# Performance work log

Hardware: AMD Instinct MI355X
Metric: run time of the kernel (lower is better)

Reference implementation:

```python
import jax, jax.numpy as jnp
import numpy as np

B, N, D, H, QP, VP = 2, 2048, 64, 4, 4, 4
DH = D // H  # 16
CUTOFF = 10.0
NEG = -1e9  # stand-in for -inf in masked_fill (identical softmax output, NaN-safe)


def _linear_params(key, din, dout):
    kw, kb = jax.random.split(key)
    W = jax.random.normal(kw, (din, dout), jnp.float32) / np.sqrt(din)
    b = jax.random.normal(kb, (dout,), jnp.float32) * 0.01
    return W, b


def setup_inputs() -> dict:
    key = jax.random.key(0)
    ks = jax.random.split(key, 10)
    features = jax.random.normal(ks[0], (B, N, D), jnp.float32)
    coords = jax.random.uniform(ks[1], (B, N, 3), jnp.float32) * 30.0  # ~protein-scale box (Angstroms)
    Wq, bq = _linear_params(ks[2], D, D)
    Wk, bk = _linear_params(ks[3], D, D)
    Wv, bv = _linear_params(ks[4], D, D)
    Wqp, bqp = _linear_params(ks[5], D, H * QP * 3)
    Wkp, bkp = _linear_params(ks[6], D, H * QP * 3)
    Wvp, bvp = _linear_params(ks[7], D, H * VP * 3)
    Wo, bo = _linear_params(ks[8], D + H * VP * 3, D)
    w_c = jnp.ones((H,), jnp.float32)
    w_l = jnp.ones((H,), jnp.float32)
    return dict(features=features, coords=coords, Wq=Wq, bq=bq, Wk=Wk, bk=bk,
                Wv=Wv, bv=bv, Wqp=Wqp, bqp=bqp, Wkp=Wkp, bkp=bkp,
                Wvp=Wvp, bvp=bvp, Wo=Wo, bo=bo, w_c=w_c, w_l=w_l)


def reference(features, coords, Wq, bq, Wk, bk, Wv, bv,
              Wqp, bqp, Wkp, bkp, Wvp, bvp, Wo, bo, w_c, w_l):
    b, n, _ = features.shape
    # cutoff edge mask (SE3Encoder: dist > cutoff is masked)
    d2 = jnp.sum((coords[:, :, None, :] - coords[:, None, :, :]) ** 2, axis=-1)  # (b,n,n)
    edge_mask = jnp.sqrt(jnp.maximum(d2, 0.0)) > CUTOFF

    q = (features @ Wq + bq).reshape(b, n, H, DH)
    k = (features @ Wk + bk).reshape(b, n, H, DH)
    v = (features @ Wv + bv).reshape(b, n, H, DH)
    qp = (features @ Wqp + bqp).reshape(b, n, H, QP, 3) + coords[:, :, None, None, :]
    kp = (features @ Wkp + bkp).reshape(b, n, H, QP, 3) + coords[:, :, None, None, :]
    vp = (features @ Wvp + bvp).reshape(b, n, H, VP, 3) + coords[:, :, None, None, :]

    linear_attn = jnp.einsum('bihd,bjhd->bhij', q, k) * (DH ** -0.5)
    # sum_{p,d} (qp - kp)^2 = |qp|^2 + |kp|^2 - 2 qp.kp, avoiding (b,n,n,H,P,3) tensor
    qsq = jnp.transpose(jnp.sum(qp ** 2, axis=(-1, -2)), (0, 2, 1))  # (b,h,i)
    ksq = jnp.transpose(jnp.sum(kp ** 2, axis=(-1, -2)), (0, 2, 1))  # (b,h,j)
    cross = jnp.einsum('bihpd,bjhpd->bhij', qp, kp)
    point_attn = -0.5 * (qsq[:, :, :, None] + ksq[:, :, None, :] - 2.0 * cross)

    wl = jax.nn.softplus(w_l)[None, :, None, None]
    wc = jax.nn.softplus(w_c)[None, :, None, None]
    attn = wl * linear_attn + wc * point_attn
    attn = jnp.where(edge_mask[:, None, :, :], NEG, attn)
    attn = jax.nn.softmax(attn, axis=-1)

    out_linear = jnp.einsum('bhij,bjhd->bihd', attn, v).reshape(b, n, -1)
    out_points = jnp.einsum('bhij,bjhpd->bihpd', attn, vp).reshape(b, n, -1)
    out = jnp.concatenate([out_linear, out_points], axis=-1)
    return out @ Wo + bo
```

## Files before the change

### kernel.cpp

```cpp
#include <hip/hip_runtime.h>
#include <hip/hip_bf16.h>

typedef __hip_bfloat16 bf16;
typedef unsigned int uint32;
typedef __attribute__((ext_vector_type(8))) short bf16x8;
typedef __attribute__((ext_vector_type(4))) float f32x4;

#define BB 2
#define NN 2048
#define CENTER 15.0f

#define QT_OFF   16u
#define KT_OFF   786448u
#define VT_OFF   1572880u
#define CQ_OFF   1802256u
#define SB_OFF   1806352u
#define PAR_OFF  2281488u

__device__ __forceinline__ float b2f(bf16 x) { return __bfloat162float(x); }

__device__ __forceinline__ float ldm(const void* p, size_t i, int mode) {
  return mode ? ((const float*)p)[i] : b2f(((const bf16*)p)[i]);
}

__device__ __forceinline__ float softplus_f(float x) {
  return (x > 20.f) ? x : log1pf(__expf(x));
}

__device__ __forceinline__ unsigned pk2(float a, float b) {
  union { __hip_bfloat162 v; unsigned u; } cv;
  cv.v.x = __float2bfloat16(a); cv.v.y = __float2bfloat16(b);
  return cv.u;
}
__device__ __forceinline__ float2 upk2(unsigned u) {
  union { unsigned u; __hip_bfloat162 v; } cv; cv.u = u;
  return make_float2(__bfloat162float(cv.v.x), __bfloat162float(cv.v.y));
}
__device__ __forceinline__ unsigned short f2bu(float x) {
  union { bf16 b; unsigned short u; } c; c.b = __float2bfloat16(x); return c.u;
}
__device__ __forceinline__ float lo_part(float x) {
  return x - __bfloat162float(__float2bfloat16(x));
}

__device__ float qslot(int h, int s, const float* spro, const float* cc,
                       float wl, float wc) {
  if (s < 16) return wl * spro[h * 16 + s];
  if (s < 28) return wc * spro[192 + h * 12 + (s - 16)];
  if (s < 32) return 0.f;
  if (s < 44) return wc * spro[192 + h * 12 + (s - 32)];
  if (s < 56) return lo_part(wc * spro[192 + h * 12 + (s - 44)]);
  if (s < 64) return 0.f;
  if (s < 67) return cc[s - 64];
  if (s < 70) return cc[s - 67];
  if (s < 73) return lo_part(cc[s - 70]);
  return 0.f;
}
__device__ float kslot(int h, int s, const float* spro, const float* cc) {
  if (s < 16) return spro[64 + h * 16 + s];
  if (s < 28) return spro[240 + h * 12 + (s - 16)];
  if (s < 32) return 0.f;
  if (s < 44) return lo_part(spro[240 + h * 12 + (s - 32)]);
  if (s < 56) return spro[240 + h * 12 + (s - 44)];
  if (s < 64) return 0.f;
  if (s < 67) return cc[s - 64];
  if (s < 70) return lo_part(cc[s - 67]);
  if (s < 73) return cc[s - 70];
  return 0.f;
}

__global__ __launch_bounds__(512) void proj_kernel(
    const void* feat, const void* coords,
    const void* Wq,  const void* bq,  const void* Wk,  const void* bk,
    const void* Wv,  const void* bv,  const void* Wqp, const void* bqp,
    const void* Wkp, const void* bkp, const void* Wvp, const void* bvp,
    const void* w_c, const void* w_l, float* ws)
{
  const int t = threadIdx.x;
  const int row0 = blockIdx.x * 4;
  const int b = row0 >> 11;
  __shared__ int scnt;
  __shared__ float sfT[64 * 4];
  __shared__ float spro[4][336];

  if (t == 0) scnt = 0;
  __syncthreads();
  {
    const unsigned short uv = ((const unsigned short*)feat)[t];
    const unsigned e = (uv >> 7) & 0xFFu;
    const unsigned long long bl = __ballot(e >= 0xC0u);
    if ((t & 63) == 0) atomicAdd(&scnt, (int)__popcll(bl));
  }
  __syncthreads();
  const int mode = (scnt > 16) ? 1 : 0;

  if (t < 256) {
    const int rr = t >> 6, f = t & 63;
    sfT[f * 4 + rr] = ldm(feat, (size_t)(row0 + rr) * 64 + f, mode);
  }
  __syncthreads();

  if (t < 336) {
    const void *W, *bias; int odim, c, cls, ofs;
    if (t < 64)       { W = Wq;  bias = bq;  odim = 64; c = t;       cls = 0; ofs = 0; }
    else if (t < 128) { W = Wk;  bias = bk;  odim = 64; c = t - 64;  cls = 1; ofs = 64; }
    else if (t < 192) { W = Wv;  bias = bv;  odim = 64; c = t - 128; cls = 2; ofs = 128; }
    else if (t < 240) { W = Wqp; bias = bqp; odim = 48; c = t - 192; cls = 3; ofs = 192; }
    else if (t < 288) { W = Wkp; bias = bkp; odim = 48; c = t - 240; cls = 4; ofs = 240; }
    else              { W = Wvp; bias = bvp; odim = 48; c = t - 288; cls = 5; ofs = 288; }
    const float bb = ldm(bias, c, mode);
    float a0 = bb, a1 = bb, a2 = bb, a3 = bb;
    if (mode) {
      const float* Wf = (const float*)W;
      #pragma unroll 8
      for (int f = 0; f < 64; ++f) {
        const float wf = Wf[(size_t)f * odim + c];
        const float4 fv = *(const float4*)(sfT + f * 4);
        a0 = fmaf(fv.x, wf, a0); a1 = fmaf(fv.y, wf, a1);
        a2 = fmaf(fv.z, wf, a2); a3 = fmaf(fv.w, wf, a3);
      }
    } else {
      const bf16* Wb = (const bf16*)W;
      #pragma unroll 8
      for (int f = 0; f < 64; ++f) {
        const float wf = b2f(Wb[(size_t)f * odim + c]);
        const float4 fv = *(const float4*)(sfT + f * 4);
        a0 = fmaf(fv.x, wf, a0); a1 = fmaf(fv.y, wf, a1);
        a2 = fmaf(fv.z, wf, a2); a3 = fmaf(fv.w, wf, a3);
      }
    }
    float av[4] = {a0, a1, a2, a3};
    #pragma unroll
    for (int rr = 0; rr < 4; ++rr) {
      float acc = av[rr];
      if (cls >= 3) {
        acc += ldm(coords, (size_t)(row0 + rr) * 3 + (c % 3), mode);
        if (cls == 3 || cls == 4) acc -= CENTER;
      }
      spro[rr][ofs + c] = acc;
    }
  }
  __syncthreads();

  if (t < 384) {
    const bool isq = (t < 192);
    const int per = isq ? t : t - 192;
    const int h = per / 48, w = per - h * 48;
    const float wl = softplus_f(ldm(w_l, h, mode)) * 0.25f;
    const float wc = softplus_f(ldm(w_c, h, mode));
    uint32* tab = (uint32*)(ws + (isq ? QT_OFF : KT_OFF));
    #pragma unroll 1
    for (int rr = 0; rr < 4; ++rr) {
      const int row = row0 + rr, i = row & 2047;
      float cc[3];
      cc[0] = ldm(coords, (size_t)row * 3 + 0, mode) - CENTER;
      cc[1] = ldm(coords, (size_t)row * 3 + 1, mode) - CENTER;
      cc[2] = ldm(coords, (size_t)row * 3 + 2, mode) - CENTER;
      const float* sp = spro[rr];
      float a0, a1;
      if (isq) { a0 = qslot(h, 2 * w, sp, cc, wl, wc);
                 a1 = qslot(h, 2 * w + 1, sp, cc, wl, wc); }
      else     { a0 = kslot(h, 2 * w, sp, cc);
                 a1 = kslot(h, 2 * w + 1, sp, cc); }
      tab[((size_t)(b * 4 + h) * NN + i) * 48 + w] = pk2(a0, a1);
    }
  } else if (t < 496) {
    const int tt = t - 384;
    const int h = tt / 28, d = tt - h * 28;
    unsigned short* VTu = (unsigned short*)(ws + VT_OFF);
    #pragma unroll 1
    for (int rr = 0; rr < 4; ++rr) {
      const int row = row0 + rr, i = row & 2047;
      const float val = (d < 16) ? spro[rr][128 + h * 16 + d]
                                 : spro[rr][288 + h * 12 + (d - 16)];
      VTu[((size_t)((b * 4 + h) * 28 + d)) * NN + i] = f2bu(val);
    }
  } else if (t < 500) {
    const int h = t - 496;
    const float wc = softplus_f(ldm(w_c, h, mode));
    #pragma unroll 1
    for (int rr = 0; rr < 4; ++rr) {
      const int row = row0 + rr, i = row & 2047;
      float s = 0.f;
      #pragma unroll
      for (int e = 0; e < 12; ++e) {
        const float y = spro[rr][240 + h * 12 + e];
        s = fmaf(y, y, s);
      }
      ws[SB_OFF + (size_t)(b * 4 + h) * NN + i] = -0.5f * wc * s;
    }
  } else if (t == 500) {
    #pragma unroll 1
    for (int rr = 0; rr < 4; ++rr) {
      const int row = row0 + rr;
      float cc[3];
      cc[0] = ldm(coords, (size_t)row * 3 + 0, mode) - CENTER;
      cc[1] = ldm(coords, (size_t)row * 3 + 1, mode) - CENTER;
      cc[2] = ldm(coords, (size_t)row * 3 + 2, mode) - CENTER;
      ws[CQ_OFF + row] = fmaf(cc[0], cc[0], fmaf(cc[1], cc[1], cc[2] * cc[2]));
    }
  }
}

__global__ __launch_bounds__(512) void attn_kernel(
    const uint32* __restrict__ QTg, const uint32* __restrict__ KTg,
    const uint32* __restrict__ VTg, const float* __restrict__ CQ,
    const float* __restrict__ SBt, float* __restrict__ parb)
{
  const int tid = threadIdx.x;
  const int lane = tid & 63;
  const int li = lane & 15, g = lane >> 4;
  const int jc = blockIdx.x;
  const int it = blockIdx.y;
  const int bh = blockIdx.z;
  const int b = bh >> 2;
  const int iloc = it * 128 + (tid >> 6) * 16 + li;
  const int j0base = jc * 512;

  const uint32* qrow = QTg + ((size_t)bh * NN + iloc) * 48;
  const bf16x8 B1 = *(const bf16x8*)(qrow + 4 * g);
  const bf16x8 B2 = *(const bf16x8*)(qrow + 16 + 4 * g);
  const bf16x8 B3 = *(const bf16x8*)(qrow + 32 + 4 * g);
  const float ciq = CQ[(size_t)b * NN + iloc];

  float m = -1e9f, l = 0.f;
  f32x4 acc0 = {0.f, 0.f, 0.f, 0.f};
  f32x4 acc1 = {0.f, 0.f, 0.f, 0.f};

  __shared__ uint32 sKT[32 * 52];
  __shared__ uint32 sVT[32 * 20];
  __shared__ float  sCS[64];

  if (tid < 80) sVT[560 + tid] = 0;

  const float4* KT4 = (const float4*)(KTg + ((size_t)bh * NN + j0base) * 48);
  const float4* VT4 = (const float4*)VTg;
  const size_t vbase = (size_t)(bh * 28) * 256 + (j0base >> 3);

  float4 kreg = {0.f, 0.f, 0.f, 0.f};
  float4 vreg = {0.f, 0.f, 0.f, 0.f};
  float  creg = 0.f;
  const int kj = tid / 12, kq = tid - kj * 12;
  const int vd = tid >> 2, vq = tid & 3;
  const int cx = tid - 448, cj = cx & 31;
  const int vA = (vq < 2) ? (8 * vq) : (8 * vq - 14);

  auto issue = [&](int jt) {
    if (tid < 384) kreg = KT4[(size_t)jt * 384 + kj * 12 + kq];
    if (tid < 112) vreg = VT4[vbase + (size_t)vd * 256 + jt * 4 + vq];
    if (tid >= 448) {
      const int jg = j0base + jt * 32 + cj;
      creg = (cx < 32) ? CQ[(size_t)b * NN + jg] : SBt[(size_t)bh * NN + jg];
    }
  };

  issue(0);

  #pragma unroll 1
  for (int jt = 0; jt < 16; ++jt) {
    if (tid < 384) *(float4*)(sKT + kj * 52 + kq * 4) = kreg;
    if (tid < 112) {
      *(float2*)(sVT + vd * 20 + vA)     = make_float2(vreg.x, vreg.y);
      *(float2*)(sVT + vd * 20 + vA + 4) = make_float2(vreg.z, vreg.w);
    }
    if (tid >= 448) sCS[(cj << 1) | (cx >> 5)] = creg;
    __syncthreads();
    if (jt < 15) issue(jt + 1);

    float s[8];
    const f32x4 z = {0.f, 0.f, 0.f, 0.f};
    __builtin_amdgcn_s_setprio(1);
    #pragma unroll
    for (int h2 = 0; h2 < 2; ++h2) {
      const uint32* arow = sKT + (h2 * 16 + li) * 52;
      const bf16x8 A1 = *(const bf16x8*)(arow + 4 * g);
      const bf16x8 A2 = *(const bf16x8*)(arow + 16 + 4 * g);
      const bf16x8 A3 = *(const bf16x8*)(arow + 32 + 4 * g);
      f32x4 Cs = __builtin_amdgcn_mfma_f32_16x16x32_bf16(A1, B1, z, 0, 0, 0);
      Cs = __builtin_amdgcn_mfma_f32_16x16x32_bf16(A2, B2, Cs, 0, 0, 0);
      const f32x4 Cd = __builtin_amdgcn_mfma_f32_16x16x32_bf16(A3, B3, z, 0, 0, 0);
      #pragma unroll
      for (int r = 0; r < 4; ++r) {
        const int jj = h2 * 16 + g * 4 + r;
        const float cjq = sCS[jj * 2], sb = sCS[jj * 2 + 1];
        const float d2 = fmaf(-2.f, Cd[r], ciq + cjq);
        const float sv = Cs[r] + sb;
        s[h2 * 4 + r] = (d2 > 100.f) ? -1e30f : sv;
      }
    }
    __builtin_amdgcn_s_setprio(0);

    float smax = fmaxf(fmaxf(fmaxf(s[0], s[1]), fmaxf(s[2], s[3])),
                       fmaxf(fmaxf(s[4], s[5]), fmaxf(s[6], s[7])));
    smax = fmaxf(smax, __shfl_xor(smax, 16));
    smax = fmaxf(smax, __shfl_xor(smax, 32));
    const float mnew = fmaxf(m, smax);
    const float alpha = __expf(m - mnew);
    m = mnew;
    l *= alpha; acc0 *= alpha; acc1 *= alpha;
    float p[8];
    #pragma unroll
    for (int k = 0; k < 8; ++k) p[k] = __expf(s[k] - m);
    l += ((p[0] + p[1]) + (p[2] + p[3])) + ((p[4] + p[5]) + (p[6] + p[7]));

    union { uint32 u[4]; bf16x8 v; } bp;
    bp.u[0] = pk2(p[0], p[1]); bp.u[1] = pk2(p[2], p[3]);
    bp.u[2] = pk2(p[4], p[5]); bp.u[3] = pk2(p[6], p[7]);

    const bf16x8 Av0 = *(const bf16x8*)(sVT + li * 20 + 4 * g);
    const bf16x8 Av1 = *(const bf16x8*)(sVT + (16 + li) * 20 + 4 * g);
    __builtin_amdgcn_s_setprio(1);
    acc0 = __builtin_amdgcn_mfma_f32_16x16x32_bf16(Av0, bp.v, acc0, 0, 0, 0);
    acc1 = __builtin_amdgcn_mfma_f32_16x16x32_bf16(Av1, bp.v, acc1, 0, 0, 0);
    __builtin_amdgcn_s_setprio(0);
    __syncthreads();
  }

  l += __shfl_xor(l, 16);
  l += __shfl_xor(l, 32);

  float* rec = parb + ((size_t)(bh * 4 + jc) * NN + iloc) * 16;
  rec[0] = m; rec[1] = l;
  uint32* ru = (uint32*)(rec + 2);
  ru[2 * g]     = pk2(acc0[0], acc0[1]);
  ru[2 * g + 1] = pk2(acc0[2], acc0[3]);
  if (g < 3) {
    ru[8 + 2 * g]     = pk2(acc1[0], acc1[1]);
    ru[8 + 2 * g + 1] = pk2(acc1[2], acc1[3]);
  }
}

__global__ __launch_bounds__(256) void out_kernel(
    const float* __restrict__ parb, const void* Wo, const void* bo,
    const unsigned short* __restrict__ ufeat, void* outp)
{
  const int t = threadIdx.x;
  const int blk = blockIdx.x;
  __shared__ int scnt;
  __shared__ float si[4 * 112];
  __shared__ float sM[16], sIL[16];

  if (t == 0) scnt = 0;
  __syncthreads();
  {
    const unsigned e = (ufeat[t] >> 7) & 0xFFu;
    const unsigned long long bl = __ballot(e >= 0xC0u);
    if ((t & 63) == 0) atomicAdd(&scnt, (int)__popcll(bl));
  }
  __syncthreads();
  const int mode = (scnt > 8) ? 1 : 0;

  if (t < 16) {
    const int lr = t >> 2, h = t & 3;
    const int row = blk * 4 + lr, b = row >> 11, i = row & 2047;
    const int bh = b * 4 + h;
    const float* base = parb + ((size_t)(bh * 4) * NN + i) * 16;
    float M = -1e9f;
    #pragma unroll
    for (int c = 0; c < 4; ++c) M = fmaxf(M, base[(size_t)c * NN * 16]);
    float L = 0.f;
    #pragma unroll
    for (int c = 0; c < 4; ++c) {
      const float* r = base + (size_t)c * NN * 16;
      L = fmaf(r[1], __expf(r[0] - M), L);
    }
    sM[t] = M; sIL[t] = 1.f / L;
  }
  __syncthreads();

  if (t < 224) {
    const int u = t / 14, pr = t - u * 14;
    const int lr = u >> 2, h = u & 3;
    const int row = blk * 4 + lr, b = row >> 11, i = row & 2047;
    const int bh = b * 4 + h;
    const float* base = parb + ((size_t)(bh * 4) * NN + i) * 16;
    const float M = sM[u], iL = sIL[u];
    float o0 = 0.f, o1 = 0.f;
    #pragma unroll
    for (int c = 0; c < 4; ++c) {
      const float* r = base + (size_t)c * NN * 16;
      const float wgt = __expf(r[0] - M);
      const float2 f = upk2(((const unsigned*)(r + 2))[pr]);
      o0 = fmaf(f.x, wgt, o0); o1 = fmaf(f.y, wgt, o1);
    }
    const int d = 2 * pr;
    const int col = (d < 16) ? (h * 16 + d) : (64 + h * 12 + (d - 16));
    si[lr * 112 + col]     = o0 * iL;
    si[lr * 112 + col + 1] = o1 * iL;
  }
  __syncthreads();

  const int lr = t >> 6, c = t & 63;
  float acc = mode ? ((const float*)bo)[c] : b2f(((const bf16*)bo)[c]);
  if (mode) {
    const float* Wf = (const float*)Wo;
    #pragma unroll 16
    for (int kk = 0; kk < 112; ++kk)
      acc = fmaf(si[lr * 112 + kk], Wf[(size_t)kk * 64 + c], acc);
  } else {
    const bf16* Wb = (const bf16*)Wo;
    #pragma unroll 16
    for (int kk = 0; kk < 112; ++kk)
      acc = fmaf(si[lr * 112 + kk], b2f(Wb[(size_t)kk * 64 + c]), acc);
  }
  const size_t oi = (size_t)(blk * 4 + lr) * 64 + c;
  if (mode) ((float*)outp)[oi] = acc;
  else      ((bf16*)outp)[oi] = __float2bfloat16(acc);
}

extern "C" void kernel_launch(void* const* d_in, const int* in_sizes, int n_in,
                              void* d_out, int out_size, void* d_ws, size_t ws_size,
                              hipStream_t stream)
{
  float* ws = (float*)d_ws;

  proj_kernel<<<BB * NN / 4, 512, 0, stream>>>(d_in[0], d_in[1], d_in[2], d_in[3],
      d_in[4], d_in[5], d_in[6], d_in[7], d_in[8], d_in[9], d_in[10], d_in[11],
      d_in[12], d_in[13], d_in[16], d_in[17], ws);

  attn_kernel<<<dim3(4, 16, 8), 512, 0, stream>>>(
      (const uint32*)(ws + QT_OFF), (const uint32*)(ws + KT_OFF),
      (const uint32*)(ws + VT_OFF), ws + CQ_OFF, ws + SB_OFF, ws + PAR_OFF);

  out_kernel<<<(BB * NN) / 4, 256, 0, stream>>>(
      ws + PAR_OFF, d_in[14], d_in[15], (const unsigned short*)d_in[0], d_out);
}
```

Measured before the change: 55.68 us.

## Double-buffer attention K/V tiles and split keys into eight chunks

The attention kernel now keeps two shared-memory buffers for the K, V and coordinate tiles. This drops one of the two barriers per iteration and lets the shared-memory write for the next tile overlap compute on the current one, with global loads prefetched two tiles ahead. The key dimension is split into 8 chunks of 256 instead of 4 chunks of 512, which doubles the grid to raise occupancy across CUs. The cost is twice as many partial softmax records in the workspace for the combine kernel to read and merge, and that larger partial buffer must still fit in the workspace.

```diff
diff --git a/kernel.cpp b/kernel.cpp
--- a/kernel.cpp
+++ b/kernel.cpp
@@ -215,7 +215,7 @@
   const int bh = blockIdx.z;
   const int b = bh >> 2;
   const int iloc = it * 128 + (tid >> 6) * 16 + li;
-  const int j0base = jc * 512;
+  const int j0base = jc * 256;
 
   const uint32* qrow = QTg + ((size_t)bh * NN + iloc) * 48;
   const bf16x8 B1 = *(const bf16x8*)(qrow + 4 * g);
@@ -227,11 +227,11 @@
   f32x4 acc0 = {0.f, 0.f, 0.f, 0.f};
   f32x4 acc1 = {0.f, 0.f, 0.f, 0.f};
 
-  __shared__ uint32 sKT[32 * 52];
-  __shared__ uint32 sVT[32 * 20];
-  __shared__ float  sCS[64];
-
-  if (tid < 80) sVT[560 + tid] = 0;
+  __shared__ uint32 sKT[2][32 * 52];
+  __shared__ uint32 sVT[2][32 * 20];
+  __shared__ float  sCS[2][64];
+
+  if (tid < 80) { sVT[0][560 + tid] = 0; sVT[1][560 + tid] = 0; }
 
   const float4* KT4 = (const float4*)(KTg + ((size_t)bh * NN + j0base) * 48);
   const float4* VT4 = (const float4*)VTg;
@@ -253,26 +253,32 @@
       creg = (cx < 32) ? CQ[(size_t)b * NN + jg] : SBt[(size_t)bh * NN + jg];
     }
   };
+  auto wr = [&](int bsel) {
+    if (tid < 384) *(float4*)(sKT[bsel] + kj * 52 + kq * 4) = kreg;
+    if (tid < 112) {
+      *(float2*)(sVT[bsel] + vd * 20 + vA)     = make_float2(vreg.x, vreg.y);
+      *(float2*)(sVT[bsel] + vd * 20 + vA + 4) = make_float2(vreg.z, vreg.w);
+    }
+    if (tid >= 448) sCS[bsel][(cj << 1) | (cx >> 5)] = creg;
+  };
 
   issue(0);
+  wr(0);
+  issue(1);
 
   #pragma unroll 1
-  for (int jt = 0; jt < 16; ++jt) {
-    if (tid < 384) *(float4*)(sKT + kj * 52 + kq * 4) = kreg;
-    if (tid < 112) {
-      *(float2*)(sVT + vd * 20 + vA)     = make_float2(vreg.x, vreg.y);
-      *(float2*)(sVT + vd * 20 + vA + 4) = make_float2(vreg.z, vreg.w);
-    }
-    if (tid >= 448) sCS[(cj << 1) | (cx >> 5)] = creg;
+  for (int jt = 0; jt < 8; ++jt) {
+    const int cur = jt & 1;
     __syncthreads();
-    if (jt < 15) issue(jt + 1);
+    if (jt + 1 < 8) wr(cur ^ 1);
+    if (jt + 2 < 8) issue(jt + 2);
 
     float s[8];
     const f32x4 z = {0.f, 0.f, 0.f, 0.f};
     __builtin_amdgcn_s_setprio(1);
     #pragma unroll
     for (int h2 = 0; h2 < 2; ++h2) {
-      const uint32* arow = sKT + (h2 * 16 + li) * 52;
+      const uint32* arow = sKT[cur] + (h2 * 16 + li) * 52;
       const bf16x8 A1 = *(const bf16x8*)(arow + 4 * g);
       const bf16x8 A2 = *(const bf16x8*)(arow + 16 + 4 * g);
       const bf16x8 A3 = *(const bf16x8*)(arow + 32 + 4 * g);
@@ -282,7 +288,7 @@
       #pragma unroll
       for (int r = 0; r < 4; ++r) {
         const int jj = h2 * 16 + g * 4 + r;
-        const float cjq = sCS[jj * 2], sb = sCS[jj * 2 + 1];
+        const float cjq = sCS[cur][jj * 2], sb = sCS[cur][jj * 2 + 1];
         const float d2 = fmaf(-2.f, Cd[r], ciq + cjq);
         const float sv = Cs[r] + sb;
         s[h2 * 4 + r] = (d2 > 100.f) ? -1e30f : sv;
@@ -307,19 +313,18 @@
     bp.u[0] = pk2(p[0], p[1]); bp.u[1] = pk2(p[2], p[3]);
     bp.u[2] = pk2(p[4], p[5]); bp.u[3] = pk2(p[6], p[7]);
 
-    const bf16x8 Av0 = *(const bf16x8*)(sVT + li * 20 + 4 * g);
-    const bf16x8 Av1 = *(const bf16x8*)(sVT + (16 + li) * 20 + 4 * g);
+    const bf16x8 Av0 = *(const bf16x8*)(sVT[cur] + li * 20 + 4 * g);
+    const bf16x8 Av1 = *(const bf16x8*)(sVT[cur] + (16 + li) * 20 + 4 * g);
     __builtin_amdgcn_s_setprio(1);
     acc0 = __builtin_amdgcn_mfma_f32_16x16x32_bf16(Av0, bp.v, acc0, 0, 0, 0);
     acc1 = __builtin_amdgcn_mfma_f32_16x16x32_bf16(Av1, bp.v, acc1, 0, 0, 0);
     __builtin_amdgcn_s_setprio(0);
-    __syncthreads();
   }
 
   l += __shfl_xor(l, 16);
   l += __shfl_xor(l, 32);
 
-  float* rec = parb + ((size_t)(bh * 4 + jc) * NN + iloc) * 16;
+  float* rec = parb + ((size_t)(bh * 8 + jc) * NN + iloc) * 16;
   rec[0] = m; rec[1] = l;
   uint32* ru = (uint32*)(rec + 2);
   ru[2 * g]     = pk2(acc0[0], acc0[1]);
@@ -354,13 +359,13 @@
     const int lr = t >> 2, h = t & 3;
     const int row = blk * 4 + lr, b = row >> 11, i = row & 2047;
     const int bh = b * 4 + h;
-    const float* base = parb + ((size_t)(bh * 4) * NN + i) * 16;
+    const float* base = parb + ((size_t)(bh * 8) * NN + i) * 16;
     float M = -1e9f;
     #pragma unroll
-    for (int c = 0; c < 4; ++c) M = fmaxf(M, base[(size_t)c * NN * 16]);
+    for (int c = 0; c < 8; ++c) M = fmaxf(M, base[(size_t)c * NN * 16]);
     float L = 0.f;
     #pragma unroll
-    for (int c = 0; c < 4; ++c) {
+    for (int c = 0; c < 8; ++c) {
       const float* r = base + (size_t)c * NN * 16;
       L = fmaf(r[1], __expf(r[0] - M), L);
     }
@@ -373,11 +378,11 @@
     const int lr = u >> 2, h = u & 3;
     const int row = blk * 4 + lr, b = row >> 11, i = row & 2047;
     const int bh = b * 4 + h;
-    const float* base = parb + ((size_t)(bh * 4) * NN + i) * 16;
+    const float* base = parb + ((size_t)(bh * 8) * NN + i) * 16;
     const float M = sM[u], iL = sIL[u];
     float o0 = 0.f, o1 = 0.f;
     #pragma unroll
-    for (int c = 0; c < 4; ++c) {
+    for (int c = 0; c < 8; ++c) {
       const float* r = base + (size_t)c * NN * 16;
       const float wgt = __expf(r[0] - M);
       const float2 f = upk2(((const unsigned*)(r + 2))[pr]);
@@ -418,7 +423,7 @@
       d_in[4], d_in[5], d_in[6], d_in[7], d_in[8], d_in[9], d_in[10], d_in[11],
       d_in[12], d_in[13], d_in[16], d_in[17], ws);
 
-  attn_kernel<<<dim3(4, 16, 8), 512, 0, stream>>>(
+  attn_kernel<<<dim3(8, 16, 8), 512, 0, stream>>>(
       (const uint32*)(ws + QT_OFF), (const uint32*)(ws + KT_OFF),
       (const uint32*)(ws + VT_OFF), ws + CQ_OFF, ws + SB_OFF, ws + PAR_OFF);
 
```

After: 60.30 us. 1.08x slower.
